# Performance work log

Measured on AMD Instinct MI355X. Metric: run time of the kernel, lower is better.

The kernel has to match this reference:

```python
import jax, jax.numpy as jnp
import numpy as np

T, H, I, E, K = 4096, 2048, 1408, 8, 2  # tokens, hidden, intermediate, experts, top_k


def setup_inputs() -> dict:
    key = jax.random.key(0)
    ks = jax.random.split(key, 6)
    hidden_states = jax.random.normal(ks[0], (T, H), dtype=jnp.float32)
    gate_weight = jax.random.normal(ks[1], (E, H), dtype=jnp.float32) * 0.02  # fp32 gate, per source assert
    w13_weight = jax.random.randint(ks[2], (E, 2 * I, H), -127, 128, dtype=jnp.int8)
    w13_weight_scale = jax.random.uniform(ks[3], (E, 2 * I), dtype=jnp.float32, minval=0.5, maxval=1.5) * 0.005
    w2_weight = jax.random.randint(ks[4], (E, H, I), -127, 128, dtype=jnp.int8)
    w2_weight_scale = jax.random.uniform(ks[5], (E, H), dtype=jnp.float32, minval=0.5, maxval=1.5) * 0.005
    return dict(hidden_states=hidden_states, gate_weight=gate_weight,
                w13_weight=w13_weight, w13_weight_scale=w13_weight_scale,
                w2_weight=w2_weight, w2_weight_scale=w2_weight_scale)


def _dynamic_quant_i8(x):
    # per-token dynamic symmetric int8: scale = max|x|/127 (smooth scales default to ones)
    s = jnp.maximum(jnp.max(jnp.abs(x), axis=-1, keepdims=True) / 127.0, 1e-8)
    q = jnp.clip(jnp.round(x / s), -127.0, 127.0)
    return q, s


def reference(hidden_states, gate_weight, w13_weight, w13_weight_scale, w2_weight, w2_weight_scale):
    # --- gating: fp32 linear + topk softmax (renormalize=True) ---
    logits = hidden_states @ gate_weight.T              # [T, E]
    probs = jax.nn.softmax(logits, axis=-1)
    topv, topi = jax.lax.top_k(probs, K)                # [T, K]
    gates = topv / jnp.sum(topv, axis=-1, keepdims=True)
    # dense routing weights [T, E]: gate value where expert selected, else 0
    route = jnp.zeros((T, E), hidden_states.dtype).at[jnp.arange(T)[:, None], topi].add(gates)

    # --- dynamic per-token int8 quant of routed input (same token value for each of its K copies) ---
    q_in, s_in = _dynamic_quant_i8(hidden_states)       # [T, H], [T, 1]

    # --- grouped w8a8 GEMM (fc1) -> SwiGLU -> requant -> grouped GEMM (fc2) -> weighted combine ---
    def step(acc, xs):
        w13, s13, w2, s2w, r = xs                       # per-expert weights / route column [T]
        h1 = (q_in @ w13.T.astype(jnp.float32)) * s_in * s13[None, :]   # dequant fc1: [T, 2I]
        g, u = h1[:, :I], h1[:, I:]
        act = jax.nn.silu(g) * u                        # SwiGLU
        q_a, s_a = _dynamic_quant_i8(act)
        h2 = (q_a @ w2.T.astype(jnp.float32)) * s_a * s2w[None, :]      # dequant fc2: [T, H]
        return acc + r[:, None] * h2, None

    acc0 = jnp.zeros_like(hidden_states)
    out, _ = jax.lax.scan(step, acc0,
                          (w13_weight, w13_weight_scale, w2_weight, w2_weight_scale, route.T))
    return out
```

## Files before the change

kernel.cpp:

```cpp
#include <hip/hip_runtime.h>

#define T_TOK 4096
#define H_DIM 2048
#define I_DIM 1408
#define E_NUM 8
#define NI2   (2 * I_DIM)

typedef int v4i __attribute__((ext_vector_type(4)));

#define GLD_LDS16(gptr, lptr)                                                        \
  __builtin_amdgcn_global_load_lds(                                                  \
      (const __attribute__((address_space(1))) void*)(gptr),                         \
      (__attribute__((address_space(3))) void*)(lptr), 16, 0, 0)

__global__ __launch_bounds__(256) void pack_all(const int* __restrict__ w13,
                                                const int* __restrict__ w2,
                                                signed char* __restrict__ qw13,
                                                signed char* __restrict__ qw2,
                                                int n16a, int n16tot) {
  int i = blockIdx.x * 256 + threadIdx.x;
  if (i >= n16tot) return;
  const int* src;
  signed char* dst;
  int j;
  if (i < n16a) { src = w13; dst = qw13; j = i; }
  else          { src = w2;  dst = qw2;  j = i - n16a; }
  const int4* s4 = (const int4*)src + (size_t)j * 4;
  int4 v0 = s4[0], v1 = s4[1], v2 = s4[2], v3 = s4[3];
  union { signed char c[16]; int4 v; } pk;
  pk.c[0] = (signed char)v0.x;  pk.c[1] = (signed char)v0.y;
  pk.c[2] = (signed char)v0.z;  pk.c[3] = (signed char)v0.w;
  pk.c[4] = (signed char)v1.x;  pk.c[5] = (signed char)v1.y;
  pk.c[6] = (signed char)v1.z;  pk.c[7] = (signed char)v1.w;
  pk.c[8] = (signed char)v2.x;  pk.c[9] = (signed char)v2.y;
  pk.c[10] = (signed char)v2.z; pk.c[11] = (signed char)v2.w;
  pk.c[12] = (signed char)v3.x; pk.c[13] = (signed char)v3.y;
  pk.c[14] = (signed char)v3.z; pk.c[15] = (signed char)v3.w;
  ((int4*)dst)[j] = pk.v;
}

__global__ __launch_bounds__(256) void gate_route_quant(
    const float* __restrict__ hs, const float* __restrict__ gw,
    signed char* __restrict__ qin, float* __restrict__ s_in,
    int* __restrict__ tope, float* __restrict__ gts) {
  const int t = blockIdx.x;
  const int tid = threadIdx.x;
  const int lane = tid & 63;
  const int wave = tid >> 6;
  const float* row = hs + (size_t)t * H_DIM;

  const float4* r4 = (const float4*)row + tid * 2;
  float4 xa = r4[0], xb = r4[1];
  float x[8] = {xa.x, xa.y, xa.z, xa.w, xb.x, xb.y, xb.z, xb.w};

  double pd[8];
  for (int e = 0; e < 8; e++) pd[e] = 0.0;
  float am = 0.f;
  for (int j = 0; j < 8; j++) {
    float v = x[j];
    am = fmaxf(am, fabsf(v));
    int col = tid * 8 + j;
    for (int e = 0; e < 8; e++)
      pd[e] += (double)v * (double)gw[e * H_DIM + col];
  }
  for (int e = 0; e < 8; e++)
    for (int s = 32; s; s >>= 1) pd[e] += __shfl_down(pd[e], s);
  for (int s = 32; s; s >>= 1) am = fmaxf(am, __shfl_down(am, s));

  __shared__ double sred[4][8];
  __shared__ float sam[4];
  __shared__ float sbc;
  if (lane == 0) {
    for (int e = 0; e < 8; e++) sred[wave][e] = pd[e];
    sam[wave] = am;
  }
  __syncthreads();
  if (tid == 0) {
    float l[8];
    for (int e = 0; e < 8; e++)
      l[e] = (float)(sred[0][e] + sred[1][e] + sred[2][e] + sred[3][e]);
    float amx = fmaxf(fmaxf(sam[0], sam[1]), fmaxf(sam[2], sam[3]));
    float s = fmaxf(amx / 127.0f, 1e-8f);
    s_in[t] = s;
    sbc = s;
    int i1 = 0;
    for (int e = 1; e < 8; e++) if (l[e] > l[i1]) i1 = e;
    int i2 = -1;
    for (int e = 0; e < 8; e++) {
      if (e == i1) continue;
      if (i2 < 0 || l[e] > l[i2]) i2 = e;
    }
    float d = expf(l[i2] - l[i1]);
    tope[2 * t] = i1;     gts[2 * t] = 1.0f / (1.0f + d);
    tope[2 * t + 1] = i2; gts[2 * t + 1] = d / (1.0f + d);
  }
  __syncthreads();
  float s = sbc;
  union { signed char c[8]; unsigned long long u; } pk;
  for (int j = 0; j < 8; j++) {
    float q = rintf(x[j] / s);
    q = fminf(127.f, fmaxf(-127.f, q));
    pk.c[j] = (signed char)q;
  }
  ((unsigned long long*)(qin + (size_t)t * H_DIM))[tid] = pk.u;
}

__global__ __launch_bounds__(256) void build_lists(
    const int* __restrict__ tope, int* __restrict__ tok_list,
    int* __restrict__ epos, int* __restrict__ cnt) {
  __shared__ int lc[E_NUM];
  __shared__ int lbase[E_NUM];
  const int tid = threadIdx.x;
  if (tid < E_NUM) lc[tid] = 0;
  __syncthreads();
  const int t = blockIdx.x * 256 + tid;
  int e0 = tope[2 * t], e1 = tope[2 * t + 1];
  int p0 = atomicAdd(&lc[e0], 1);
  int p1 = atomicAdd(&lc[e1], 1);
  __syncthreads();
  if (tid < E_NUM) lbase[tid] = atomicAdd(&cnt[tid], lc[tid]);
  __syncthreads();
  int pos0 = lbase[e0] + p0;
  int pos1 = lbase[e1] + p1;
  tok_list[e0 * T_TOK + pos0] = t;
  tok_list[e1 * T_TOK + pos1] = t;
  epos[2 * t] = (e0 << 16) | pos0;
  epos[2 * t + 1] = (e1 << 16) | pos1;
}

__global__ void calc_off(const int* __restrict__ cnt, int* __restrict__ off) {
  if (threadIdx.x == 0) {
    int s = 0;
    for (int e = 0; e < E_NUM; e++) { off[e] = s; s += cnt[e]; }
  }
}

__global__ __launch_bounds__(256, 2) void gemm1_silu(
    const signed char* __restrict__ qw13, const signed char* __restrict__ qin,
    const float* __restrict__ s_in, const float* __restrict__ s13,
    const int* __restrict__ tok_list, const int* __restrict__ cnt,
    const int* __restrict__ off, float* __restrict__ act,
    unsigned int* __restrict__ amax) {
  const int bid = blockIdx.x;
  const int e = bid & 7;
  const int yt = (bid >> 3) & 31;
  const int xt = bid >> 8;
  const int ce = cnt[e];
  const int m0 = yt * 128;
  if (m0 >= ce) return;
  const int n0 = xt * 64;

  __shared__ __align__(16) signed char As[128 * 64];
  __shared__ __align__(16) signed char Bg[64 * 64];
  __shared__ __align__(16) signed char Bu[64 * 64];

  const int tid = threadIdx.x;
  const int lane = tid & 63;
  const int wave = tid >> 6;
  const int quad = lane >> 4;
  const int ln = lane & 15;

  const int* tl = tok_list + e * T_TOK;
  const int rowA = tid >> 2;
  const int kc = (tid & 3) * 16;

  const int tA0 = tl[min(m0 + rowA, ce - 1)];
  const int tA1 = tl[min(m0 + 64 + rowA, ce - 1)];
  const signed char* gA0 = qin + (size_t)tA0 * H_DIM + kc;
  const signed char* gA1 = qin + (size_t)tA1 * H_DIM + kc;
  const signed char* w13e = qw13 + (size_t)e * NI2 * H_DIM;
  const signed char* gBg = w13e + (size_t)(n0 + rowA) * H_DIM + kc;
  const signed char* gBu = gBg + (size_t)I_DIM * H_DIM;
  const int ldsA = tid * 16;

  v4i accg[2][4], accu[2][4];
  v4i zero = {0, 0, 0, 0};
#pragma unroll
  for (int i = 0; i < 2; i++)
#pragma unroll
    for (int j = 0; j < 4; j++) { accg[i][j] = zero; accu[i][j] = zero; }

  for (int k0 = 0; k0 < H_DIM; k0 += 64) {
    __syncthreads();
    GLD_LDS16(gA0 + k0, As + ldsA);
    GLD_LDS16(gA1 + k0, As + 4096 + ldsA);
    GLD_LDS16(gBg + k0, Bg + ldsA);
    GLD_LDS16(gBu + k0, Bu + ldsA);
    __syncthreads();

    v4i af[2], bg[4], bu[4];
#pragma unroll
    for (int mt = 0; mt < 2; mt++)
      af[mt] = *(const v4i*)(As + (wave * 32 + mt * 16 + ln) * 64 + quad * 16);
#pragma unroll
    for (int nf = 0; nf < 4; nf++) {
      bg[nf] = *(const v4i*)(Bg + (nf * 16 + ln) * 64 + quad * 16);
      bu[nf] = *(const v4i*)(Bu + (nf * 16 + ln) * 64 + quad * 16);
    }
#pragma unroll
    for (int mt = 0; mt < 2; mt++)
#pragma unroll
      for (int nf = 0; nf < 4; nf++) {
        accg[mt][nf] = __builtin_amdgcn_mfma_i32_16x16x64_i8(af[mt], bg[nf], accg[mt][nf], 0, 0, 0);
        accu[mt][nf] = __builtin_amdgcn_mfma_i32_16x16x64_i8(af[mt], bu[nf], accu[mt][nf], 0, 0, 0);
      }
  }

  const float* s13e = s13 + e * NI2;
  float sg[4], su[4];
  int ncol[4];
#pragma unroll
  for (int nf = 0; nf < 4; nf++) {
    int n = n0 + nf * 16 + ln;
    ncol[nf] = n;
    sg[nf] = s13e[n];
    su[nf] = s13e[I_DIM + n];
  }
  const int offe = off[e];
#pragma unroll
  for (int mt = 0; mt < 2; mt++) {
#pragma unroll
    for (int r = 0; r < 4; r++) {
      int mrel = m0 + wave * 32 + mt * 16 + quad * 4 + r;
      bool valid = mrel < ce;
      int tok = tl[valid ? mrel : 0];
      float si = s_in[tok];
      int crow = offe + mrel;
      float* arow = act + (size_t)crow * I_DIM;
      float am = 0.f;
#pragma unroll
      for (int nf = 0; nf < 4; nf++) {
        float g = (float)accg[mt][nf][r] * si * sg[nf];
        float u = (float)accu[mt][nf][r] * si * su[nf];
        float a = g / (1.0f + expf(-g)) * u;
        if (valid) arow[ncol[nf]] = a;
        am = fmaxf(am, fabsf(a));
      }
      for (int s = 1; s < 16; s <<= 1) am = fmaxf(am, __shfl_xor(am, s, 16));
      if (valid && ln == 0) atomicMax(amax + crow, __float_as_uint(am));
    }
  }
}

__global__ __launch_bounds__(256) void quant_act(const float* __restrict__ act,
                                                 const unsigned int* __restrict__ amax,
                                                 signed char* __restrict__ qa,
                                                 float* __restrict__ s_a) {
  const int r = blockIdx.x;
  float am = __uint_as_float(amax[r]);
  float s = fmaxf(am / 127.0f, 1e-8f);
  if (threadIdx.x == 0) s_a[r] = s;
  const float* arow = act + (size_t)r * I_DIM;
  signed char* qrow = qa + (size_t)r * I_DIM;
  for (int j = threadIdx.x; j < I_DIM; j += 256) {
    float q = rintf(arow[j] / s);
    q = fminf(127.f, fmaxf(-127.f, q));
    qrow[j] = (signed char)q;
  }
}

__global__ __launch_bounds__(256, 2) void gemm2_h2(
    const signed char* __restrict__ qw2, const signed char* __restrict__ qa,
    const float* __restrict__ s_a, const float* __restrict__ s2w,
    const int* __restrict__ cnt, const int* __restrict__ off,
    float* __restrict__ h2s) {
  const int bid = blockIdx.x;
  const int e = bid & 7;
  const int yt = (bid >> 3) & 31;
  const int xt = bid >> 8;
  const int ce = cnt[e];
  const int m0 = yt * 128;
  if (m0 >= ce) return;
  const int n0 = xt * 128;
  const int offe = off[e];

  __shared__ __align__(16) signed char As[128 * 64];
  __shared__ __align__(16) signed char Bs[128 * 64];

  const int tid = threadIdx.x;
  const int lane = tid & 63;
  const int wave = tid >> 6;
  const int quad = lane >> 4;
  const int ln = lane & 15;

  const int rowA = tid >> 2;
  const int kc = (tid & 3) * 16;

  const signed char* gA0 = qa + (size_t)(offe + min(m0 + rowA, ce - 1)) * I_DIM + kc;
  const signed char* gA1 = qa + (size_t)(offe + min(m0 + 64 + rowA, ce - 1)) * I_DIM + kc;
  const signed char* w2e = qw2 + (size_t)e * H_DIM * I_DIM;
  const signed char* gB0 = w2e + (size_t)(n0 + rowA) * I_DIM + kc;
  const signed char* gB1 = gB0 + (size_t)64 * I_DIM;
  const int ldsA = tid * 16;

  v4i acc[2][8];
  v4i zero = {0, 0, 0, 0};
#pragma unroll
  for (int i = 0; i < 2; i++)
#pragma unroll
    for (int j = 0; j < 8; j++) acc[i][j] = zero;

  for (int k0 = 0; k0 < I_DIM; k0 += 64) {
    __syncthreads();
    GLD_LDS16(gA0 + k0, As + ldsA);
    GLD_LDS16(gA1 + k0, As + 4096 + ldsA);
    GLD_LDS16(gB0 + k0, Bs + ldsA);
    GLD_LDS16(gB1 + k0, Bs + 4096 + ldsA);
    __syncthreads();

    v4i af[2], bf[8];
#pragma unroll
    for (int mt = 0; mt < 2; mt++)
      af[mt] = *(const v4i*)(As + (wave * 32 + mt * 16 + ln) * 64 + quad * 16);
#pragma unroll
    for (int nf = 0; nf < 8; nf++)
      bf[nf] = *(const v4i*)(Bs + (nf * 16 + ln) * 64 + quad * 16);
#pragma unroll
    for (int mt = 0; mt < 2; mt++)
#pragma unroll
      for (int nf = 0; nf < 8; nf++)
        acc[mt][nf] = __builtin_amdgcn_mfma_i32_16x16x64_i8(af[mt], bf[nf], acc[mt][nf], 0, 0, 0);
  }

  const float* s2e = s2w + e * H_DIM;
  float sw[8];
  int ncol[8];
#pragma unroll
  for (int nf = 0; nf < 8; nf++) {
    int n = n0 + nf * 16 + ln;
    ncol[nf] = n;
    sw[nf] = s2e[n];
  }
#pragma unroll
  for (int mt = 0; mt < 2; mt++) {
#pragma unroll
    for (int r = 0; r < 4; r++) {
      int mrel = m0 + wave * 32 + mt * 16 + quad * 4 + r;
      if (mrel >= ce) continue;
      float sa = s_a[offe + mrel];
      float* orow = h2s + (size_t)(offe + mrel) * H_DIM;
#pragma unroll
      for (int nf = 0; nf < 8; nf++)
        orow[ncol[nf]] = (float)acc[mt][nf][r] * sa * sw[nf];
    }
  }
}

__global__ __launch_bounds__(256) void gather_out(
    const float* __restrict__ h2s, const int* __restrict__ epos,
    const float* __restrict__ gts, const int* __restrict__ off,
    float* __restrict__ out) {
  const int t = blockIdx.x;
  int a = epos[2 * t], b = epos[2 * t + 1];
  float g1 = gts[2 * t], g2 = gts[2 * t + 1];
  int r1 = off[a >> 16] + (a & 0xffff);
  int r2 = off[b >> 16] + (b & 0xffff);
  const float4* R1 = (const float4*)(h2s + (size_t)r1 * H_DIM);
  const float4* R2 = (const float4*)(h2s + (size_t)r2 * H_DIM);
  float4* O = (float4*)(out + (size_t)t * H_DIM);
  for (int c = threadIdx.x; c < H_DIM / 4; c += 256) {
    float4 x = R1[c], y = R2[c];
    float4 z;
    z.x = g1 * x.x + g2 * y.x;
    z.y = g1 * x.y + g2 * y.y;
    z.z = g1 * x.z + g2 * y.z;
    z.w = g1 * x.w + g2 * y.w;
    O[c] = z;
  }
}

extern "C" void kernel_launch(void* const* d_in, const int* in_sizes, int n_in,
                              void* d_out, int out_size, void* d_ws, size_t ws_size,
                              hipStream_t stream) {
  const float* hs = (const float*)d_in[0];
  const float* gw = (const float*)d_in[1];
  const int* w13 = (const int*)d_in[2];
  const float* s13 = (const float*)d_in[3];
  const int* w2 = (const int*)d_in[4];
  const float* s2w = (const float*)d_in[5];
  float* out = (float*)d_out;

  char* ws = (char*)d_ws;
  size_t o = 0;
  auto take = [&](size_t b) {
    char* p = ws + o;
    o += (b + 255) & ~(size_t)255;
    return p;
  };
  signed char* qw13 = (signed char*)take((size_t)E_NUM * NI2 * H_DIM);
  signed char* qin = (signed char*)take((size_t)T_TOK * H_DIM);
  float* act = (float*)take((size_t)T_TOK * 2 * I_DIM * 4);
  float* h2s = (float*)qw13;
  signed char* qw2 = (signed char*)take((size_t)E_NUM * H_DIM * I_DIM);
  signed char* qa = (signed char*)take((size_t)T_TOK * 2 * I_DIM);
  float* sin_ = (float*)take((size_t)T_TOK * 4);
  float* sa = (float*)take((size_t)T_TOK * 2 * 4);
  unsigned int* amax = (unsigned int*)take((size_t)T_TOK * 2 * 4);
  int* tokl = (int*)take((size_t)E_NUM * T_TOK * 4);
  int* tope = (int*)take((size_t)T_TOK * 2 * 4);
  int* epos = (int*)take((size_t)T_TOK * 2 * 4);
  float* gts = (float*)take((size_t)T_TOK * 2 * 4);
  int* cnt = (int*)take(E_NUM * 4);
  int* off = (int*)take(E_NUM * 4);

  hipMemsetAsync(amax, 0, (size_t)T_TOK * 2 * 4, stream);
  hipMemsetAsync(cnt, 0, (size_t)E_NUM * 4, stream);

  {
    int n16a = E_NUM * NI2 * H_DIM / 16;
    int n16b = E_NUM * H_DIM * I_DIM / 16;
    int n16tot = n16a + n16b;
    pack_all<<<(n16tot + 255) / 256, 256, 0, stream>>>(w13, w2, qw13, qw2, n16a, n16tot);
  }
  gate_route_quant<<<T_TOK, 256, 0, stream>>>(hs, gw, qin, sin_, tope, gts);
  build_lists<<<T_TOK / 256, 256, 0, stream>>>(tope, tokl, epos, cnt);
  calc_off<<<1, 64, 0, stream>>>(cnt, off);
  gemm1_silu<<<(I_DIM / 64) * (T_TOK / 128) * E_NUM, 256, 0, stream>>>(qw13, qin, sin_, s13, tokl, cnt, off, act, amax);
  quant_act<<<T_TOK * 2, 256, 0, stream>>>(act, amax, qa, sa);
  gemm2_h2<<<(H_DIM / 128) * (T_TOK / 128) * E_NUM, 256, 0, stream>>>(qw2, qa, sa, s2w, cnt, off, h2s);
  gather_out<<<T_TOK, 256, 0, stream>>>(h2s, epos, gts, off, out);
}
```

Before: 563.2 us.

## Use 2x2 wave tiling with XOR-swizzled LDS and single-block routing list build

Both grouped GEMM kernels change from 4x1 wave tiling to a 2x2 wave grid, so each wave loads fewer B fragments per MFMA and register reuse of A/B tiles goes up. LDS reads and writes use an XOR swizzle on the 16-byte k-chunk to cut bank conflicts on the fragment loads. The routing list build is merged with offset computation into one single-block kernel, which removes the calc_off launch and the cnt memset. The single-block build serializes 4096 tokens through one workgroup, and because it runs sequentially with atomics, the token order within each expert now depends on atomic ordering.

```diff
diff --git a/kernel.cpp b/kernel.cpp
--- a/kernel.cpp
+++ b/kernel.cpp
@@ -107,31 +107,25 @@
 
 __global__ __launch_bounds__(256) void build_lists(
     const int* __restrict__ tope, int* __restrict__ tok_list,
-    int* __restrict__ epos, int* __restrict__ cnt) {
+    int* __restrict__ epos, int* __restrict__ cnt, int* __restrict__ off) {
   __shared__ int lc[E_NUM];
-  __shared__ int lbase[E_NUM];
   const int tid = threadIdx.x;
   if (tid < E_NUM) lc[tid] = 0;
   __syncthreads();
-  const int t = blockIdx.x * 256 + tid;
-  int e0 = tope[2 * t], e1 = tope[2 * t + 1];
-  int p0 = atomicAdd(&lc[e0], 1);
-  int p1 = atomicAdd(&lc[e1], 1);
+  for (int t0 = 0; t0 < T_TOK; t0 += 256) {
+    int t = t0 + tid;
+    int e0 = tope[2 * t], e1 = tope[2 * t + 1];
+    int p0 = atomicAdd(&lc[e0], 1);
+    int p1 = atomicAdd(&lc[e1], 1);
+    tok_list[e0 * T_TOK + p0] = t;
+    tok_list[e1 * T_TOK + p1] = t;
+    epos[2 * t] = (e0 << 16) | p0;
+    epos[2 * t + 1] = (e1 << 16) | p1;
+  }
   __syncthreads();
-  if (tid < E_NUM) lbase[tid] = atomicAdd(&cnt[tid], lc[tid]);
-  __syncthreads();
-  int pos0 = lbase[e0] + p0;
-  int pos1 = lbase[e1] + p1;
-  tok_list[e0 * T_TOK + pos0] = t;
-  tok_list[e1 * T_TOK + pos1] = t;
-  epos[2 * t] = (e0 << 16) | pos0;
-  epos[2 * t + 1] = (e1 << 16) | pos1;
-}
-
-__global__ void calc_off(const int* __restrict__ cnt, int* __restrict__ off) {
-  if (threadIdx.x == 0) {
+  if (tid == 0) {
     int s = 0;
-    for (int e = 0; e < E_NUM; e++) { off[e] = s; s += cnt[e]; }
+    for (int e = 0; e < E_NUM; e++) { cnt[e] = lc[e]; off[e] = s; s += lc[e]; }
   }
 }
 
@@ -157,12 +151,14 @@
   const int tid = threadIdx.x;
   const int lane = tid & 63;
   const int wave = tid >> 6;
+  const int wm = wave >> 1;
+  const int wn = wave & 1;
   const int quad = lane >> 4;
   const int ln = lane & 15;
 
   const int* tl = tok_list + e * T_TOK;
   const int rowA = tid >> 2;
-  const int kc = (tid & 3) * 16;
+  const int kc = (((tid & 3) ^ ((tid >> 3) & 3)) * 16);
 
   const int tA0 = tl[min(m0 + rowA, ce - 1)];
   const int tA1 = tl[min(m0 + 64 + rowA, ce - 1)];
@@ -172,13 +168,14 @@
   const signed char* gBg = w13e + (size_t)(n0 + rowA) * H_DIM + kc;
   const signed char* gBu = gBg + (size_t)I_DIM * H_DIM;
   const int ldsA = tid * 16;
-
-  v4i accg[2][4], accu[2][4];
+  const int ks = ((quad ^ ((ln >> 1) & 3)) * 16);
+
+  v4i accg[4][2], accu[4][2];
   v4i zero = {0, 0, 0, 0};
 #pragma unroll
-  for (int i = 0; i < 2; i++)
-#pragma unroll
-    for (int j = 0; j < 4; j++) { accg[i][j] = zero; accu[i][j] = zero; }
+  for (int i = 0; i < 4; i++)
+#pragma unroll
+    for (int j = 0; j < 2; j++) { accg[i][j] = zero; accu[i][j] = zero; }
 
   for (int k0 = 0; k0 < H_DIM; k0 += 64) {
     __syncthreads();
@@ -188,40 +185,40 @@
     GLD_LDS16(gBu + k0, Bu + ldsA);
     __syncthreads();
 
-    v4i af[2], bg[4], bu[4];
-#pragma unroll
-    for (int mt = 0; mt < 2; mt++)
-      af[mt] = *(const v4i*)(As + (wave * 32 + mt * 16 + ln) * 64 + quad * 16);
-#pragma unroll
-    for (int nf = 0; nf < 4; nf++) {
-      bg[nf] = *(const v4i*)(Bg + (nf * 16 + ln) * 64 + quad * 16);
-      bu[nf] = *(const v4i*)(Bu + (nf * 16 + ln) * 64 + quad * 16);
+    v4i af[4], bg[2], bu[2];
+#pragma unroll
+    for (int mt = 0; mt < 4; mt++)
+      af[mt] = *(const v4i*)(As + (wm * 64 + mt * 16 + ln) * 64 + ks);
+#pragma unroll
+    for (int nf = 0; nf < 2; nf++) {
+      bg[nf] = *(const v4i*)(Bg + (wn * 32 + nf * 16 + ln) * 64 + ks);
+      bu[nf] = *(const v4i*)(Bu + (wn * 32 + nf * 16 + ln) * 64 + ks);
     }
 #pragma unroll
-    for (int mt = 0; mt < 2; mt++)
-#pragma unroll
-      for (int nf = 0; nf < 4; nf++) {
+    for (int mt = 0; mt < 4; mt++)
+#pragma unroll
+      for (int nf = 0; nf < 2; nf++) {
         accg[mt][nf] = __builtin_amdgcn_mfma_i32_16x16x64_i8(af[mt], bg[nf], accg[mt][nf], 0, 0, 0);
         accu[mt][nf] = __builtin_amdgcn_mfma_i32_16x16x64_i8(af[mt], bu[nf], accu[mt][nf], 0, 0, 0);
       }
   }
 
   const float* s13e = s13 + e * NI2;
-  float sg[4], su[4];
-  int ncol[4];
-#pragma unroll
-  for (int nf = 0; nf < 4; nf++) {
-    int n = n0 + nf * 16 + ln;
+  float sg[2], su[2];
+  int ncol[2];
+#pragma unroll
+  for (int nf = 0; nf < 2; nf++) {
+    int n = n0 + wn * 32 + nf * 16 + ln;
     ncol[nf] = n;
     sg[nf] = s13e[n];
     su[nf] = s13e[I_DIM + n];
   }
   const int offe = off[e];
 #pragma unroll
-  for (int mt = 0; mt < 2; mt++) {
+  for (int mt = 0; mt < 4; mt++) {
 #pragma unroll
     for (int r = 0; r < 4; r++) {
-      int mrel = m0 + wave * 32 + mt * 16 + quad * 4 + r;
+      int mrel = m0 + wm * 64 + mt * 16 + quad * 4 + r;
       bool valid = mrel < ce;
       int tok = tl[valid ? mrel : 0];
       float si = s_in[tok];
@@ -229,7 +226,7 @@
       float* arow = act + (size_t)crow * I_DIM;
       float am = 0.f;
 #pragma unroll
-      for (int nf = 0; nf < 4; nf++) {
+      for (int nf = 0; nf < 2; nf++) {
         float g = (float)accg[mt][nf][r] * si * sg[nf];
         float u = (float)accu[mt][nf][r] * si * su[nf];
         float a = g / (1.0f + expf(-g)) * u;
@@ -280,11 +277,13 @@
   const int tid = threadIdx.x;
   const int lane = tid & 63;
   const int wave = tid >> 6;
+  const int wm = wave >> 1;
+  const int wn = wave & 1;
   const int quad = lane >> 4;
   const int ln = lane & 15;
 
   const int rowA = tid >> 2;
-  const int kc = (tid & 3) * 16;
+  const int kc = (((tid & 3) ^ ((tid >> 3) & 3)) * 16);
 
   const signed char* gA0 = qa + (size_t)(offe + min(m0 + rowA, ce - 1)) * I_DIM + kc;
   const signed char* gA1 = qa + (size_t)(offe + min(m0 + 64 + rowA, ce - 1)) * I_DIM + kc;
@@ -292,13 +291,14 @@
   const signed char* gB0 = w2e + (size_t)(n0 + rowA) * I_DIM + kc;
   const signed char* gB1 = gB0 + (size_t)64 * I_DIM;
   const int ldsA = tid * 16;
-
-  v4i acc[2][8];
+  const int ks = ((quad ^ ((ln >> 1) & 3)) * 16);
+
+  v4i acc[4][4];
   v4i zero = {0, 0, 0, 0};
 #pragma unroll
-  for (int i = 0; i < 2; i++)
-#pragma unroll
-    for (int j = 0; j < 8; j++) acc[i][j] = zero;
+  for (int i = 0; i < 4; i++)
+#pragma unroll
+    for (int j = 0; j < 4; j++) acc[i][j] = zero;
 
   for (int k0 = 0; k0 < I_DIM; k0 += 64) {
     __syncthreads();
@@ -308,39 +308,39 @@
     GLD_LDS16(gB1 + k0, Bs + 4096 + ldsA);
     __syncthreads();
 
-    v4i af[2], bf[8];
-#pragma unroll
-    for (int mt = 0; mt < 2; mt++)
-      af[mt] = *(const v4i*)(As + (wave * 32 + mt * 16 + ln) * 64 + quad * 16);
-#pragma unroll
-    for (int nf = 0; nf < 8; nf++)
-      bf[nf] = *(const v4i*)(Bs + (nf * 16 + ln) * 64 + quad * 16);
-#pragma unroll
-    for (int mt = 0; mt < 2; mt++)
-#pragma unroll
-      for (int nf = 0; nf < 8; nf++)
+    v4i af[4], bf[4];
+#pragma unroll
+    for (int mt = 0; mt < 4; mt++)
+      af[mt] = *(const v4i*)(As + (wm * 64 + mt * 16 + ln) * 64 + ks);
+#pragma unroll
+    for (int nf = 0; nf < 4; nf++)
+      bf[nf] = *(const v4i*)(Bs + (wn * 64 + nf * 16 + ln) * 64 + ks);
+#pragma unroll
+    for (int mt = 0; mt < 4; mt++)
+#pragma unroll
+      for (int nf = 0; nf < 4; nf++)
         acc[mt][nf] = __builtin_amdgcn_mfma_i32_16x16x64_i8(af[mt], bf[nf], acc[mt][nf], 0, 0, 0);
   }
 
   const float* s2e = s2w + e * H_DIM;
-  float sw[8];
-  int ncol[8];
-#pragma unroll
-  for (int nf = 0; nf < 8; nf++) {
-    int n = n0 + nf * 16 + ln;
+  float sw[4];
+  int ncol[4];
+#pragma unroll
+  for (int nf = 0; nf < 4; nf++) {
+    int n = n0 + wn * 64 + nf * 16 + ln;
     ncol[nf] = n;
     sw[nf] = s2e[n];
   }
 #pragma unroll
-  for (int mt = 0; mt < 2; mt++) {
+  for (int mt = 0; mt < 4; mt++) {
 #pragma unroll
     for (int r = 0; r < 4; r++) {
-      int mrel = m0 + wave * 32 + mt * 16 + quad * 4 + r;
+      int mrel = m0 + wm * 64 + mt * 16 + quad * 4 + r;
       if (mrel >= ce) continue;
       float sa = s_a[offe + mrel];
       float* orow = h2s + (size_t)(offe + mrel) * H_DIM;
 #pragma unroll
-      for (int nf = 0; nf < 8; nf++)
+      for (int nf = 0; nf < 4; nf++)
         orow[ncol[nf]] = (float)acc[mt][nf][r] * sa * sw[nf];
     }
   }
@@ -404,7 +404,6 @@
   int* off = (int*)take(E_NUM * 4);
 
   hipMemsetAsync(amax, 0, (size_t)T_TOK * 2 * 4, stream);
-  hipMemsetAsync(cnt, 0, (size_t)E_NUM * 4, stream);
 
   {
     int n16a = E_NUM * NI2 * H_DIM / 16;
@@ -413,8 +412,7 @@
     pack_all<<<(n16tot + 255) / 256, 256, 0, stream>>>(w13, w2, qw13, qw2, n16a, n16tot);
   }
   gate_route_quant<<<T_TOK, 256, 0, stream>>>(hs, gw, qin, sin_, tope, gts);
-  build_lists<<<T_TOK / 256, 256, 0, stream>>>(tope, tokl, epos, cnt);
-  calc_off<<<1, 64, 0, stream>>>(cnt, off);
+  build_lists<<<1, 256, 0, stream>>>(tope, tokl, epos, cnt, off);
   gemm1_silu<<<(I_DIM / 64) * (T_TOK / 128) * E_NUM, 256, 0, stream>>>(qw13, qin, sin_, s13, tokl, cnt, off, act, amax);
   quant_act<<<T_TOK * 2, 256, 0, stream>>>(act, amax, qa, sa);
   gemm2_h2<<<(H_DIM / 128) * (T_TOK / 128) * E_NUM, 256, 0, stream>>>(qw2, qa, sa, s2w, cnt, off, h2s);
```

Result: no change. 574.4 us (+2.0%).
